# Kernel optimization log

Hardware: AMD Instinct MI355X
Metric: run time of the kernel (lower is better)

Reference implementation:

```python
import jax, jax.numpy as jnp
import numpy as np

P_IN = 32  # MODEL_CONFIG['p_in']; note: all 32 sample points share the same offsets in the source


def _bilinear_border(feat, sx, sy):
    """Replicates F.grid_sample(mode='bilinear', padding_mode='border', align_corners=False)
    for a single point per (b, n). feat: [B,C,H,W]; sx, sy: [B,N] in pixel coords.
    align_corners=False unnormalization of grid built as 2*s/size - 1 gives px = s - 0.5.
    Returns [B,N,C]."""
    H, W = feat.shape[-2], feat.shape[-1]
    px = jnp.clip(sx - 0.5, 0.0, W - 1.0)  # border padding clamps coords
    py = jnp.clip(sy - 0.5, 0.0, H - 1.0)
    x0 = jnp.floor(px)
    y0 = jnp.floor(py)
    wx = (px - x0)[..., None]  # [B,N,1]
    wy = (py - y0)[..., None]
    x0i = x0.astype(jnp.int32)
    y0i = y0.astype(jnp.int32)
    x1i = jnp.minimum(x0i + 1, W - 1)
    y1i = jnp.minimum(y0i + 1, H - 1)

    def gather(f, yi, xi):  # f [C,H,W], yi/xi [N] -> [N,C]
        return f[:, yi, xi].T

    g = jax.vmap(gather)  # over batch
    v00 = g(feat, y0i, x0i)
    v01 = g(feat, y0i, x1i)
    v10 = g(feat, y1i, x0i)
    v11 = g(feat, y1i, x1i)
    return (v00 * (1 - wx) * (1 - wy) + v01 * wx * (1 - wy)
            + v10 * (1 - wx) * wy + v11 * wx * wy)


def _forward(feats, query_pos, query_content, W_off, b_off, sigma_z):
    offsets = query_content @ W_off + b_off  # [B,N,3]
    x, y, z, r = (query_pos[..., i] for i in range(4))
    dx, dy, dz = offsets[..., 0], offsets[..., 1], offsets[..., 2]
    sx = x + dx * (2.0 ** (z - r))
    sy = y + dy * (2.0 ** (z + r))
    sz = z + dz
    L = len(feats)
    levels = jnp.arange(L, dtype=sz.dtype)
    # gaussian z weight, then softmax over levels (as in source: softmax of the exp values)
    w = jnp.exp(-((sz[..., None] - levels) ** 2) / (2.0 * sigma_z ** 2))  # [B,N,L]
    zw = jax.nn.softmax(w, axis=-1)
    out = sum(zw[..., l:l + 1] * _bilinear_border(feats[l], sx, sy) for l in range(L))  # [B,N,C]
    B, N, C = out.shape
    # all P_IN sample points use identical coords in the source -> broadcast
    return jnp.broadcast_to(out[:, :, None, :], (B, N, P_IN, C))


def setup_inputs() -> dict:
    key = jax.random.key(0)
    ks = jax.random.split(key, 8)
    B, N, C = 8, 300, 256
    sizes = [(100, 100), (50, 50), (25, 25), (13, 13)]
    feats = [jax.random.normal(ks[i], (B, C, h, w), dtype=jnp.float32)
             for i, (h, w) in enumerate(sizes)]
    u = jax.random.uniform(ks[4], (B, N, 4), dtype=jnp.float32)
    # x in [0,100), y in [0,100) (level-0 pixel coords), z in [0,4), r in [0,1)
    query_pos = u * jnp.array([100.0, 100.0, 4.0, 1.0], dtype=jnp.float32)
    query_content = jax.random.normal(ks[5], (B, N, C), dtype=jnp.float32)
    W_off = jax.random.normal(ks[6], (C, 3), dtype=jnp.float32) * 0.02
    b_off = jnp.zeros((3,), dtype=jnp.float32)
    sigma_z = jnp.ones((1,), dtype=jnp.float32) * 0.5
    return {"feat0": feats[0], "feat1": feats[1], "feat2": feats[2], "feat3": feats[3],
            "query_pos": query_pos, "query_content": query_content,
            "W_off": W_off, "b_off": b_off, "sigma_z": sigma_z}


def reference(feat0, feat1, feat2, feat3, query_pos, query_content, W_off, b_off, sigma_z):
    return _forward([feat0, feat1, feat2, feat3], query_pos, query_content, W_off, b_off, sigma_z)
```

## Files before the change

kernel.cpp:

```cpp
#include <hip/hip_runtime.h>

constexpr int Bc = 8;
constexpr int Nc = 300;
constexpr int Cc = 256;
constexpr int Pc = 32;

typedef float f32x4 __attribute__((ext_vector_type(4)));

constexpr int LVL_OFF[4] = {0, 10000, 12500, 13125};
constexpr int LDS_FLOATS = 13294;

__device__ __forceinline__ void gl_lds16(const void* g, void* l) {
    __builtin_amdgcn_global_load_lds(
        (const __attribute__((address_space(1))) void*)g,
        (__attribute__((address_space(3))) void*)l, 16, 0, 0);
}
__device__ __forceinline__ void gl_lds4(const void* g, void* l) {
    __builtin_amdgcn_global_load_lds(
        (const __attribute__((address_space(1))) void*)g,
        (__attribute__((address_space(3))) void*)l, 4, 0, 0);
}

__global__ __launch_bounds__(256) void params_kernel(
    const float* __restrict__ qpos, const float* __restrict__ qcont,
    const float* __restrict__ Woff, const float* __restrict__ boff,
    const float* __restrict__ sigma, float* __restrict__ params)
{
    const int q = blockIdx.x;
    const int c = threadIdx.x;
    float qc = qcont[q * Cc + c];
    float p0 = qc * Woff[c * 3 + 0];
    float p1 = qc * Woff[c * 3 + 1];
    float p2 = qc * Woff[c * 3 + 2];
#pragma unroll
    for (int off = 32; off > 0; off >>= 1) {
        p0 += __shfl_down(p0, off, 64);
        p1 += __shfl_down(p1, off, 64);
        p2 += __shfl_down(p2, off, 64);
    }
    __shared__ float red[4][3];
    const int wave = threadIdx.x >> 6;
    if ((threadIdx.x & 63) == 0) {
        red[wave][0] = p0; red[wave][1] = p1; red[wave][2] = p2;
    }
    __syncthreads();
    if (threadIdx.x == 0) {
        float dx = red[0][0] + red[1][0] + red[2][0] + red[3][0] + boff[0];
        float dy = red[0][1] + red[1][1] + red[2][1] + red[3][1] + boff[1];
        float dz = red[0][2] + red[1][2] + red[2][2] + red[3][2] + boff[2];
        float x = qpos[q * 4 + 0];
        float y = qpos[q * 4 + 1];
        float z = qpos[q * 4 + 2];
        float r = qpos[q * 4 + 3];
        float sx = x + dx * exp2f(z - r);
        float sy = y + dy * exp2f(z + r);
        float sz = z + dz;
        float sg = sigma[0];
        float inv = 1.0f / (2.0f * sg * sg);
        float e[4];
        float s = 0.f;
#pragma unroll
        for (int l = 0; l < 4; ++l) {
            float d = sz - (float)l;
            float w = __expf(-d * d * inv);
            e[l] = __expf(w);
            s += e[l];
        }
        float rs = 1.0f / s;
        params[q * 8 + 0] = sx;
        params[q * 8 + 1] = sy;
#pragma unroll
        for (int l = 0; l < 4; ++l) params[q * 8 + 2 + l] = e[l] * rs;
    }
}

__device__ __forceinline__ float lerp_lds(const float* __restrict__ base, int W,
                                          float sx, float sy)
{
    float px = fminf(fmaxf(sx - 0.5f, 0.f), (float)(W - 1));
    float py = fminf(fmaxf(sy - 0.5f, 0.f), (float)(W - 1));
    float x0f = floorf(px);
    float y0f = floorf(py);
    float wx = px - x0f;
    float wy = py - y0f;
    int x0 = (int)x0f;
    int y0 = (int)y0f;
    int x1 = min(x0 + 1, W - 1);
    int y1 = min(y0 + 1, W - 1);
    float v00 = base[y0 * W + x0];
    float v01 = base[y0 * W + x1];
    float v10 = base[y1 * W + x0];
    float v11 = base[y1 * W + x1];
    float top = v00 + wx * (v01 - v00);
    float bot = v10 + wx * (v11 - v10);
    return top + wy * (bot - top);
}

__global__ __launch_bounds__(256) void sample_kernel(
    const float* __restrict__ f0, const float* __restrict__ f1,
    const float* __restrict__ f2, const float* __restrict__ f3,
    const float* __restrict__ params, float* __restrict__ outT)
{
    __shared__ float sl[LDS_FLOATS];
    const int bc = blockIdx.x;
    const int t = threadIdx.x;
    const int b = bc >> 8;
    const int wave = t >> 6;
    const int lane = t & 63;

    const int q0 = b * Nc + t;
    const bool has2 = (t < Nc - 256);
    const int q1 = q0 + 256;
    float sx0 = params[q0 * 8 + 0];
    float sy0 = params[q0 * 8 + 1];
    float zw0_0 = params[q0 * 8 + 2], zw0_1 = params[q0 * 8 + 3];
    float zw0_2 = params[q0 * 8 + 4], zw0_3 = params[q0 * 8 + 5];
    float sx1 = 0.f, sy1 = 0.f, zw1_0 = 0.f, zw1_1 = 0.f, zw1_2 = 0.f, zw1_3 = 0.f;
    if (has2) {
        sx1 = params[q1 * 8 + 0];
        sy1 = params[q1 * 8 + 1];
        zw1_0 = params[q1 * 8 + 2]; zw1_1 = params[q1 * 8 + 3];
        zw1_2 = params[q1 * 8 + 4]; zw1_3 = params[q1 * 8 + 5];
    }

    {
        const char* g0 = (const char*)(f0 + (size_t)bc * 10000);
        char* l0 = (char*)&sl[LVL_OFF[0]];
        for (int i = wave; i < 39; i += 4)
            gl_lds16(g0 + i * 1024 + lane * 16, l0 + i * 1024);
        if (wave == 3 && lane < 4)
            gl_lds16(g0 + 39 * 1024 + lane * 16, l0 + 39 * 1024);
    }
    {
        const char* g1 = (const char*)(f1 + (size_t)bc * 2500);
        char* l1 = (char*)&sl[LVL_OFF[1]];
        for (int i = wave; i < 9; i += 4)
            gl_lds16(g1 + i * 1024 + lane * 16, l1 + i * 1024);
        if (wave == 2 && lane < 49)
            gl_lds16(g1 + 9 * 1024 + lane * 16, l1 + 9 * 1024);
    }
    {
        const char* g2 = (const char*)(f2 + (size_t)bc * 625);
        char* l2 = (char*)&sl[LVL_OFF[2]];
        for (int i = wave; i < 9; i += 4)
            gl_lds4(g2 + i * 256 + lane * 4, l2 + i * 256);
        if (wave == 1 && lane < 49)
            gl_lds4(g2 + 9 * 256 + lane * 4, l2 + 9 * 256);
    }
    {
        const char* g3 = (const char*)(f3 + (size_t)bc * 169);
        char* l3 = (char*)&sl[LVL_OFF[3]];
        for (int i = wave; i < 2; i += 4)
            gl_lds4(g3 + i * 256 + lane * 4, l3 + i * 256);
        if (wave == 3 && lane < 41)
            gl_lds4(g3 + 2 * 256 + lane * 4, l3 + 2 * 256);
    }
    __syncthreads();

    {
        float acc = zw0_0 * lerp_lds(&sl[LVL_OFF[0]], 100, sx0, sy0)
                  + zw0_1 * lerp_lds(&sl[LVL_OFF[1]],  50, sx0, sy0)
                  + zw0_2 * lerp_lds(&sl[LVL_OFF[2]],  25, sx0, sy0)
                  + zw0_3 * lerp_lds(&sl[LVL_OFF[3]],  13, sx0, sy0);
        outT[(size_t)bc * Nc + t] = acc;
    }
    if (has2) {
        float acc = zw1_0 * lerp_lds(&sl[LVL_OFF[0]], 100, sx1, sy1)
                  + zw1_1 * lerp_lds(&sl[LVL_OFF[1]],  50, sx1, sy1)
                  + zw1_2 * lerp_lds(&sl[LVL_OFF[2]],  25, sx1, sy1)
                  + zw1_3 * lerp_lds(&sl[LVL_OFF[3]],  13, sx1, sy1);
        outT[(size_t)bc * Nc + t + 256] = acc;
    }
}

__global__ __launch_bounds__(256) void broadcast_kernel(
    const float* __restrict__ outT, float* __restrict__ out)
{
    __shared__ float sval[Cc];
    const int q = blockIdx.x;
    const int b = q / Nc;
    const int n = q - b * Nc;
    const int c = threadIdx.x;
    sval[c] = outT[((size_t)(b * Cc + c)) * Nc + n];
    __syncthreads();

    const int wave = threadIdx.x >> 6;
    const int c4 = (threadIdx.x & 63) * 4;
    f32x4 val = *(const f32x4*)&sval[c4];
    float* obase = out + (size_t)q * (Pc * Cc) + c4;
#pragma unroll
    for (int p = wave; p < Pc; p += 4) {
        __builtin_nontemporal_store(val, (f32x4*)(obase + p * Cc));
    }
}

__global__ __launch_bounds__(256) void sampling3d_fallback(
    const float* __restrict__ f0, const float* __restrict__ f1,
    const float* __restrict__ f2, const float* __restrict__ f3,
    const float* __restrict__ qpos, const float* __restrict__ qcont,
    const float* __restrict__ Woff, const float* __restrict__ boff,
    const float* __restrict__ sigma, float* __restrict__ out)
{
    const int q = blockIdx.x;
    const int b = q / Nc;
    const int c = threadIdx.x;
    float qc = qcont[q * Cc + c];
    float p0 = qc * Woff[c * 3 + 0];
    float p1 = qc * Woff[c * 3 + 1];
    float p2 = qc * Woff[c * 3 + 2];
#pragma unroll
    for (int off = 32; off > 0; off >>= 1) {
        p0 += __shfl_down(p0, off, 64);
        p1 += __shfl_down(p1, off, 64);
        p2 += __shfl_down(p2, off, 64);
    }
    __shared__ float red[4][3];
    __shared__ float par[8];
    __shared__ float accs[Cc];
    const int wave = threadIdx.x >> 6;
    if ((threadIdx.x & 63) == 0) { red[wave][0] = p0; red[wave][1] = p1; red[wave][2] = p2; }
    __syncthreads();
    if (threadIdx.x == 0) {
        float dx = red[0][0] + red[1][0] + red[2][0] + red[3][0] + boff[0];
        float dy = red[0][1] + red[1][1] + red[2][1] + red[3][1] + boff[1];
        float dz = red[0][2] + red[1][2] + red[2][2] + red[3][2] + boff[2];
        float x = qpos[q * 4 + 0], y = qpos[q * 4 + 1];
        float z = qpos[q * 4 + 2], r = qpos[q * 4 + 3];
        float sx = x + dx * exp2f(z - r);
        float sy = y + dy * exp2f(z + r);
        float sz = z + dz;
        float sg = sigma[0];
        float inv = 1.0f / (2.0f * sg * sg);
        float e[4]; float s = 0.f;
#pragma unroll
        for (int l = 0; l < 4; ++l) {
            float d = sz - (float)l;
            float w = __expf(-d * d * inv);
            e[l] = __expf(w);
            s += e[l];
        }
        float rs = 1.0f / s;
        par[0] = sx; par[1] = sy;
#pragma unroll
        for (int l = 0; l < 4; ++l) par[2 + l] = e[l] * rs;
    }
    __syncthreads();
    const float sx = par[0];
    const float sy = par[1];
    const float* const fs[4] = {f0, f1, f2, f3};
    const int HWs[4] = {100, 50, 25, 13};
    float acc = 0.f;
#pragma unroll
    for (int l = 0; l < 4; ++l) {
        const int W = HWs[l];
        float px = fminf(fmaxf(sx - 0.5f, 0.f), (float)(W - 1));
        float py = fminf(fmaxf(sy - 0.5f, 0.f), (float)(W - 1));
        float x0f = floorf(px), y0f = floorf(py);
        float wx = px - x0f, wy = py - y0f;
        int x0 = (int)x0f, y0 = (int)y0f;
        int x1 = min(x0 + 1, W - 1), y1 = min(y0 + 1, W - 1);
        const float* base = fs[l] + (size_t)((b * Cc + c) * W) * W;
        float v00 = base[y0 * W + x0];
        float v01 = base[y0 * W + x1];
        float v10 = base[y1 * W + x0];
        float v11 = base[y1 * W + x1];
        float top = v00 + wx * (v01 - v00);
        float bot = v10 + wx * (v11 - v10);
        acc += par[2 + l] * (top + wy * (bot - top));
    }
    accs[c] = acc;
    __syncthreads();
    const int c4 = (threadIdx.x & 63) * 4;
    f32x4 val = *(const f32x4*)&accs[c4];
    float* obase = out + (size_t)q * (Pc * Cc) + c4;
#pragma unroll
    for (int p = wave; p < Pc; p += 4) {
        __builtin_nontemporal_store(val, (f32x4*)(obase + p * Cc));
    }
}

extern "C" void kernel_launch(void* const* d_in, const int* in_sizes, int n_in,
                              void* d_out, int out_size, void* d_ws, size_t ws_size,
                              hipStream_t stream) {
    const float* f0    = (const float*)d_in[0];
    const float* f1    = (const float*)d_in[1];
    const float* f2    = (const float*)d_in[2];
    const float* f3    = (const float*)d_in[3];
    const float* qpos  = (const float*)d_in[4];
    const float* qcont = (const float*)d_in[5];
    const float* Woff  = (const float*)d_in[6];
    const float* boff  = (const float*)d_in[7];
    const float* sigma = (const float*)d_in[8];
    float* out = (float*)d_out;

    const size_t params_bytes = (size_t)Bc * Nc * 8 * sizeof(float);
    const size_t outT_bytes   = (size_t)Bc * Cc * Nc * sizeof(float);

    if (ws_size >= params_bytes + outT_bytes) {
        float* params = (float*)d_ws;
        float* outT   = (float*)((char*)d_ws + params_bytes);
        params_kernel<<<Bc * Nc, 256, 0, stream>>>(qpos, qcont, Woff, boff, sigma, params);
        sample_kernel<<<Bc * Cc, 256, 0, stream>>>(f0, f1, f2, f3, params, outT);
        broadcast_kernel<<<Bc * Nc, 256, 0, stream>>>(outT, out);
    } else {
        sampling3d_fallback<<<Bc * Nc, 256, 0, stream>>>(
            f0, f1, f2, f3, qpos, qcont, Woff, boff, sigma, out);
    }
}
```

Baseline: 191.1 us.

## Double-buffer feature slices in sample kernel and pack four queries per params block

The sample kernel now handles four channel slices per block. It keeps two LDS buffers and issues the async global-to-LDS load for the next slice while it interpolates the current one, so load latency overlaps with compute. The params kernel now gives each query one wavefront and packs four queries per block, which removes the cross-wave LDS reduction and barrier. In exchange the sample kernel uses about twice the LDS per block and launches a quarter as many blocks, which lowers occupancy and may expose latency.

```diff
diff --git a/kernel.cpp b/kernel.cpp
--- a/kernel.cpp
+++ b/kernel.cpp
@@ -8,7 +8,7 @@
 typedef float f32x4 __attribute__((ext_vector_type(4)));
 
 constexpr int LVL_OFF[4] = {0, 10000, 12500, 13125};
-constexpr int LDS_FLOATS = 13294;
+constexpr int SLICE_FLOATS = 13294;
 
 __device__ __forceinline__ void gl_lds16(const void* g, void* l) {
     __builtin_amdgcn_global_load_lds(
@@ -26,28 +26,29 @@
     const float* __restrict__ Woff, const float* __restrict__ boff,
     const float* __restrict__ sigma, float* __restrict__ params)
 {
-    const int q = blockIdx.x;
-    const int c = threadIdx.x;
-    float qc = qcont[q * Cc + c];
-    float p0 = qc * Woff[c * 3 + 0];
-    float p1 = qc * Woff[c * 3 + 1];
-    float p2 = qc * Woff[c * 3 + 2];
+    const int w = threadIdx.x >> 6;
+    const int lane = threadIdx.x & 63;
+    const int q = blockIdx.x * 4 + w;
+
+    f32x4 qc = *(const f32x4*)&qcont[(size_t)q * Cc + lane * 4];
+    float p0 = 0.f, p1 = 0.f, p2 = 0.f;
+#pragma unroll
+    for (int j = 0; j < 4; ++j) {
+        const float* wr = &Woff[(lane * 4 + j) * 3];
+        p0 += qc[j] * wr[0];
+        p1 += qc[j] * wr[1];
+        p2 += qc[j] * wr[2];
+    }
 #pragma unroll
     for (int off = 32; off > 0; off >>= 1) {
         p0 += __shfl_down(p0, off, 64);
         p1 += __shfl_down(p1, off, 64);
         p2 += __shfl_down(p2, off, 64);
     }
-    __shared__ float red[4][3];
-    const int wave = threadIdx.x >> 6;
-    if ((threadIdx.x & 63) == 0) {
-        red[wave][0] = p0; red[wave][1] = p1; red[wave][2] = p2;
-    }
-    __syncthreads();
-    if (threadIdx.x == 0) {
-        float dx = red[0][0] + red[1][0] + red[2][0] + red[3][0] + boff[0];
-        float dy = red[0][1] + red[1][1] + red[2][1] + red[3][1] + boff[1];
-        float dz = red[0][2] + red[1][2] + red[2][2] + red[3][2] + boff[2];
+    if (lane == 0) {
+        float dx = p0 + boff[0];
+        float dy = p1 + boff[1];
+        float dz = p2 + boff[2];
         float x = qpos[q * 4 + 0];
         float y = qpos[q * 4 + 1];
         float z = qpos[q * 4 + 2];
@@ -62,8 +63,8 @@
 #pragma unroll
         for (int l = 0; l < 4; ++l) {
             float d = sz - (float)l;
-            float w = __expf(-d * d * inv);
-            e[l] = __expf(w);
+            float wgt = __expf(-d * d * inv);
+            e[l] = __expf(wgt);
             s += e[l];
         }
         float rs = 1.0f / s;
@@ -96,17 +97,56 @@
     return top + wy * (bot - top);
 }
 
+__device__ __forceinline__ void issue_slice_dma(
+    const float* __restrict__ f0, const float* __restrict__ f1,
+    const float* __restrict__ f2, const float* __restrict__ f3,
+    int bc, float* __restrict__ buf, int wave, int lane)
+{
+    {
+        const char* g0 = (const char*)(f0 + (size_t)bc * 10000);
+        char* l0 = (char*)&buf[LVL_OFF[0]];
+        for (int i = wave; i < 39; i += 4)
+            gl_lds16(g0 + i * 1024 + lane * 16, l0 + i * 1024);
+        if (wave == 3 && lane < 4)
+            gl_lds16(g0 + 39 * 1024 + lane * 16, l0 + 39 * 1024);
+    }
+    {
+        const char* g1 = (const char*)(f1 + (size_t)bc * 2500);
+        char* l1 = (char*)&buf[LVL_OFF[1]];
+        for (int i = wave; i < 9; i += 4)
+            gl_lds16(g1 + i * 1024 + lane * 16, l1 + i * 1024);
+        if (wave == 2 && lane < 49)
+            gl_lds16(g1 + 9 * 1024 + lane * 16, l1 + 9 * 1024);
+    }
+    {
+        const char* g2 = (const char*)(f2 + (size_t)bc * 625);
+        char* l2 = (char*)&buf[LVL_OFF[2]];
+        for (int i = wave; i < 9; i += 4)
+            gl_lds4(g2 + i * 256 + lane * 4, l2 + i * 256);
+        if (wave == 1 && lane < 49)
+            gl_lds4(g2 + 9 * 256 + lane * 4, l2 + 9 * 256);
+    }
+    {
+        const char* g3 = (const char*)(f3 + (size_t)bc * 169);
+        char* l3 = (char*)&buf[LVL_OFF[3]];
+        for (int i = wave; i < 2; i += 4)
+            gl_lds4(g3 + i * 256 + lane * 4, l3 + i * 256);
+        if (wave == 3 && lane < 41)
+            gl_lds4(g3 + 2 * 256 + lane * 4, l3 + 2 * 256);
+    }
+}
+
 __global__ __launch_bounds__(256) void sample_kernel(
     const float* __restrict__ f0, const float* __restrict__ f1,
     const float* __restrict__ f2, const float* __restrict__ f3,
     const float* __restrict__ params, float* __restrict__ outT)
 {
-    __shared__ float sl[LDS_FLOATS];
-    const int bc = blockIdx.x;
+    __shared__ float sl[2][SLICE_FLOATS];
     const int t = threadIdx.x;
-    const int b = bc >> 8;
     const int wave = t >> 6;
     const int lane = t & 63;
+    const int bc0 = blockIdx.x * 4;
+    const int b = bc0 >> 8;
 
     const int q0 = b * Nc + t;
     const bool has2 = (t < Nc - 256);
@@ -123,53 +163,29 @@
         zw1_2 = params[q1 * 8 + 4]; zw1_3 = params[q1 * 8 + 5];
     }
 
-    {
-        const char* g0 = (const char*)(f0 + (size_t)bc * 10000);
-        char* l0 = (char*)&sl[LVL_OFF[0]];
-        for (int i = wave; i < 39; i += 4)
-            gl_lds16(g0 + i * 1024 + lane * 16, l0 + i * 1024);
-        if (wave == 3 && lane < 4)
-            gl_lds16(g0 + 39 * 1024 + lane * 16, l0 + 39 * 1024);
-    }
-    {
-        const char* g1 = (const char*)(f1 + (size_t)bc * 2500);
-        char* l1 = (char*)&sl[LVL_OFF[1]];
-        for (int i = wave; i < 9; i += 4)
-            gl_lds16(g1 + i * 1024 + lane * 16, l1 + i * 1024);
-        if (wave == 2 && lane < 49)
-            gl_lds16(g1 + 9 * 1024 + lane * 16, l1 + 9 * 1024);
-    }
-    {
-        const char* g2 = (const char*)(f2 + (size_t)bc * 625);
-        char* l2 = (char*)&sl[LVL_OFF[2]];
-        for (int i = wave; i < 9; i += 4)
-            gl_lds4(g2 + i * 256 + lane * 4, l2 + i * 256);
-        if (wave == 1 && lane < 49)
-            gl_lds4(g2 + 9 * 256 + lane * 4, l2 + 9 * 256);
-    }
-    {
-        const char* g3 = (const char*)(f3 + (size_t)bc * 169);
-        char* l3 = (char*)&sl[LVL_OFF[3]];
-        for (int i = wave; i < 2; i += 4)
-            gl_lds4(g3 + i * 256 + lane * 4, l3 + i * 256);
-        if (wave == 3 && lane < 41)
-            gl_lds4(g3 + 2 * 256 + lane * 4, l3 + 2 * 256);
-    }
-    __syncthreads();
-
-    {
-        float acc = zw0_0 * lerp_lds(&sl[LVL_OFF[0]], 100, sx0, sy0)
-                  + zw0_1 * lerp_lds(&sl[LVL_OFF[1]],  50, sx0, sy0)
-                  + zw0_2 * lerp_lds(&sl[LVL_OFF[2]],  25, sx0, sy0)
-                  + zw0_3 * lerp_lds(&sl[LVL_OFF[3]],  13, sx0, sy0);
-        outT[(size_t)bc * Nc + t] = acc;
-    }
-    if (has2) {
-        float acc = zw1_0 * lerp_lds(&sl[LVL_OFF[0]], 100, sx1, sy1)
-                  + zw1_1 * lerp_lds(&sl[LVL_OFF[1]],  50, sx1, sy1)
-                  + zw1_2 * lerp_lds(&sl[LVL_OFF[2]],  25, sx1, sy1)
-                  + zw1_3 * lerp_lds(&sl[LVL_OFF[3]],  13, sx1, sy1);
-        outT[(size_t)bc * Nc + t + 256] = acc;
+    issue_slice_dma(f0, f1, f2, f3, bc0, sl[0], wave, lane);
+#pragma unroll
+    for (int k = 0; k < 4; ++k) {
+        __syncthreads();
+        if (k + 1 < 4)
+            issue_slice_dma(f0, f1, f2, f3, bc0 + k + 1, sl[(k + 1) & 1], wave, lane);
+
+        const float* buf = sl[k & 1];
+        const int bc = bc0 + k;
+        {
+            float acc = zw0_0 * lerp_lds(&buf[LVL_OFF[0]], 100, sx0, sy0)
+                      + zw0_1 * lerp_lds(&buf[LVL_OFF[1]],  50, sx0, sy0)
+                      + zw0_2 * lerp_lds(&buf[LVL_OFF[2]],  25, sx0, sy0)
+                      + zw0_3 * lerp_lds(&buf[LVL_OFF[3]],  13, sx0, sy0);
+            outT[(size_t)bc * Nc + t] = acc;
+        }
+        if (has2) {
+            float acc = zw1_0 * lerp_lds(&buf[LVL_OFF[0]], 100, sx1, sy1)
+                      + zw1_1 * lerp_lds(&buf[LVL_OFF[1]],  50, sx1, sy1)
+                      + zw1_2 * lerp_lds(&buf[LVL_OFF[2]],  25, sx1, sy1)
+                      + zw1_3 * lerp_lds(&buf[LVL_OFF[3]],  13, sx1, sy1);
+            outT[(size_t)bc * Nc + t + 256] = acc;
+        }
     }
 }
 
@@ -299,8 +315,8 @@
     if (ws_size >= params_bytes + outT_bytes) {
         float* params = (float*)d_ws;
         float* outT   = (float*)((char*)d_ws + params_bytes);
-        params_kernel<<<Bc * Nc, 256, 0, stream>>>(qpos, qcont, Woff, boff, sigma, params);
-        sample_kernel<<<Bc * Cc, 256, 0, stream>>>(f0, f1, f2, f3, params, outT);
+        params_kernel<<<Bc * Nc / 4, 256, 0, stream>>>(qpos, qcont, Woff, boff, sigma, params);
+        sample_kernel<<<Bc * Cc / 4, 256, 0, stream>>>(f0, f1, f2, f3, params, outT);
         broadcast_kernel<<<Bc * Nc, 256, 0, stream>>>(outT, out);
     } else {
         sampling3d_fallback<<<Bc * Nc, 256, 0, stream>>>(
```

Result: no change. 191.3 us (+0.1%).
